# Performance work log

Measured on AMD Instinct MI355X. Metric: run time of the kernel, lower is better.

Reference implementation:

```python
import jax, jax.numpy as jnp
import numpy as np

COMMITMENT_COST = 0.25


def setup_inputs() -> dict:
    key = jax.random.key(0)
    k1, k2 = jax.random.split(key)
    B, S, D, K = 64, 512, 512, 4096
    inputs = jax.random.normal(k1, (B, S, D), dtype=jnp.float32)
    # codebook initialized uniform(-1/K, 1/K) like the torch module
    codebook = jax.random.uniform(k2, (K, D), dtype=jnp.float32,
                                  minval=-1.0 / K, maxval=1.0 / K)
    return {"inputs": inputs, "codebook": codebook}


def reference(inputs, codebook):
    D = inputs.shape[-1]
    flat = inputs.reshape(-1, D)  # [N, D]
    # squared euclidean distances to every code: [N, K]
    dist = (jnp.sum(flat * flat, axis=1, keepdims=True)
            + jnp.sum(codebook * codebook, axis=1)
            - 2.0 * flat @ codebook.T)
    idx = jnp.argmin(dist, axis=1)  # [N]
    # gather replaces one-hot scatter + matmul (same math)
    quantized = codebook[idx].reshape(inputs.shape)
    commitment_loss = jnp.mean((jax.lax.stop_gradient(quantized) - inputs) ** 2)
    codebook_loss = jnp.mean((quantized - jax.lax.stop_gradient(inputs)) ** 2)
    quantize_loss = COMMITMENT_COST * commitment_loss + codebook_loss
    # straight-through estimator
    quantized_st = inputs + jax.lax.stop_gradient(quantized - inputs)
    encoding_indices = idx.reshape(inputs.shape[:-1])
    return quantized_st, quantize_loss, encoding_indices
```

## Files before the change

kernel.cpp:

```cpp
#include <hip/hip_runtime.h>

#define N_ROWS 32768
#define DIM    512
#define KCODES 4096
#define NPARTS 4
#define KPART  (KCODES / NPARTS)
#define Q_ELEMS (N_ROWS * DIM)
#define LOSS_OFF Q_ELEMS
#define IDX_OFF (Q_ELEMS + 1)

__global__ void k_cnorm(const float* __restrict__ cb, float* __restrict__ cnorm) {
    int wave = (blockIdx.x * blockDim.x + threadIdx.x) >> 6;
    int lane = threadIdx.x & 63;
    if (wave >= KCODES) return;
    const float4* row = (const float4*)(cb + (size_t)wave * DIM);
    float4 v1 = row[lane];
    float4 v2 = row[lane + 64];
    float s = v1.x*v1.x + v1.y*v1.y + v1.z*v1.z + v1.w*v1.w
            + v2.x*v2.x + v2.y*v2.y + v2.z*v2.z + v2.w*v2.w;
    #pragma unroll
    for (int m = 32; m >= 1; m >>= 1) s += __shfl_xor(s, m);
    if (lane == 0) cnorm[wave] = s;
}

__global__ void k_xnorm(const float* __restrict__ x, float* __restrict__ xnorm) {
    int wave = (blockIdx.x * blockDim.x + threadIdx.x) >> 6;
    int lane = threadIdx.x & 63;
    if (wave >= N_ROWS) return;
    const float4* row = (const float4*)(x + (size_t)wave * DIM);
    float4 v1 = row[lane];
    float4 v2 = row[lane + 64];
    float s = v1.x*v1.x + v1.y*v1.y + v1.z*v1.z + v1.w*v1.w
            + v2.x*v2.x + v2.y*v2.y + v2.z*v2.z + v2.w*v2.w;
    #pragma unroll
    for (int m = 32; m >= 1; m >>= 1) s += __shfl_xor(s, m);
    if (lane == 0) xnorm[wave] = s;
}

#define BM 64
#define BN 128
#define BD 32
#define NCH ((KPART / BN) * (DIM / BD))

__global__ __launch_bounds__(256)
void k_argmin(const float* __restrict__ x, const float* __restrict__ cb,
              const float* __restrict__ cnorm, const float* __restrict__ xnorm,
              float* __restrict__ bestv, int* __restrict__ bestk) {
    __shared__ float xs[BM][BD + 4];
    __shared__ float cs[BD][BN];

    const int tid = threadIdx.x;
    const int ty = tid >> 4;
    const int tx = tid & 15;
    const int r0 = blockIdx.x * BM;
    const int kbase = blockIdx.y * KPART;

    const int xrow1 = tid >> 3;
    const int xrow2 = (tid + 256) >> 3;
    const int xdq   = tid & 7;
    const int ck    = tid & 127;
    const int cdq0  = tid >> 7;

    float xn[4];
    #pragma unroll
    for (int i = 0; i < 4; ++i) xn[i] = xnorm[r0 + ty * 4 + i];

    float best[4];
    int   bidx[4];
    #pragma unroll
    for (int i = 0; i < 4; ++i) { best[i] = 3.4e38f; bidx[i] = kbase; }

    float acc[4][8];
    float4 xr0, xr1, cr[4];

    xr0 = *(const float4*)(x + (size_t)(r0 + xrow1) * DIM + xdq * 4);
    xr1 = *(const float4*)(x + (size_t)(r0 + xrow2) * DIM + xdq * 4);
    #pragma unroll
    for (int it2 = 0; it2 < 4; ++it2) {
        int dq = cdq0 + it2 * 2;
        cr[it2] = *(const float4*)(cb + (size_t)(kbase + ck) * DIM + dq * 4);
    }

    #pragma unroll 1
    for (int it = 0; it < NCH; ++it) {
        const int kc = it >> 4;

        __syncthreads();
        *(float4*)&xs[xrow1][xdq * 4] = xr0;
        *(float4*)&xs[xrow2][xdq * 4] = xr1;
        #pragma unroll
        for (int it2 = 0; it2 < 4; ++it2) {
            int dq = cdq0 + it2 * 2;
            cs[dq * 4 + 0][ck] = cr[it2].x;
            cs[dq * 4 + 1][ck] = cr[it2].y;
            cs[dq * 4 + 2][ck] = cr[it2].z;
            cs[dq * 4 + 3][ck] = cr[it2].w;
        }
        __syncthreads();

        if (it + 1 < NCH) {
            const int nkc = (it + 1) >> 4;
            const int ndc = ((it + 1) & 15) * BD;
            xr0 = *(const float4*)(x + (size_t)(r0 + xrow1) * DIM + ndc + xdq * 4);
            xr1 = *(const float4*)(x + (size_t)(r0 + xrow2) * DIM + ndc + xdq * 4);
            #pragma unroll
            for (int it2 = 0; it2 < 4; ++it2) {
                int dq = cdq0 + it2 * 2;
                cr[it2] = *(const float4*)(cb + (size_t)(kbase + nkc * BN + ck) * DIM + ndc + dq * 4);
            }
        }

        if ((it & 15) == 0) {
            #pragma unroll
            for (int i = 0; i < 4; ++i)
                #pragma unroll
                for (int j = 0; j < 8; ++j) acc[i][j] = 0.f;
        }

        #pragma unroll
        for (int d4 = 0; d4 < 8; ++d4) {
            float xa[4][4];
            #pragma unroll
            for (int i = 0; i < 4; ++i)
                *(float4*)&xa[i][0] = *(const float4*)&xs[ty * 4 + i][d4 * 4];
            #pragma unroll
            for (int dd = 0; dd < 4; ++dd) {
                int d = d4 * 4 + dd;
                float4 b0 = *(const float4*)&cs[d][tx * 4];
                float4 b1 = *(const float4*)&cs[d][64 + tx * 4];
                #pragma unroll
                for (int i = 0; i < 4; ++i) {
                    float a = xa[i][dd];
                    acc[i][0] = fmaf(a, b0.x, acc[i][0]);
                    acc[i][1] = fmaf(a, b0.y, acc[i][1]);
                    acc[i][2] = fmaf(a, b0.z, acc[i][2]);
                    acc[i][3] = fmaf(a, b0.w, acc[i][3]);
                    acc[i][4] = fmaf(a, b1.x, acc[i][4]);
                    acc[i][5] = fmaf(a, b1.y, acc[i][5]);
                    acc[i][6] = fmaf(a, b1.z, acc[i][6]);
                    acc[i][7] = fmaf(a, b1.w, acc[i][7]);
                }
            }
        }

        if ((it & 15) == 15) {
            #pragma unroll
            for (int half = 0; half < 2; ++half) {
                #pragma unroll
                for (int j = 0; j < 4; ++j) {
                    int k = kbase + kc * BN + half * 64 + tx * 4 + j;
                    float cn = cnorm[k];
                    #pragma unroll
                    for (int i = 0; i < 4; ++i) {
                        float t1 = xn[i] + cn;
                        float tw = 2.0f * acc[i][half * 4 + j];
                        float s  = t1 - tw;
                        if (s < best[i]) { best[i] = s; bidx[i] = k; }
                    }
                }
            }
        }
    }

    #pragma unroll
    for (int i = 0; i < 4; ++i) {
        float b = best[i];
        int   ix = bidx[i];
        #pragma unroll
        for (int m = 1; m <= 8; m <<= 1) {
            float ob = __shfl_xor(b, m);
            int   oi = __shfl_xor(ix, m);
            if (ob < b || (ob == b && oi < ix)) { b = ob; ix = oi; }
        }
        if (tx == 0) {
            int row = r0 + ty * 4 + i;
            bestv[(size_t)blockIdx.y * N_ROWS + row] = b;
            bestk[(size_t)blockIdx.y * N_ROWS + row] = ix;
        }
    }
}

__global__ void k_gather(const float* __restrict__ x, const float* __restrict__ cb,
                         const float* __restrict__ bestv, const int* __restrict__ bestk,
                         float* __restrict__ qout, float* __restrict__ idx_out,
                         float* __restrict__ partial) {
    int row  = blockIdx.x * 4 + (threadIdx.x >> 6);
    int lane = threadIdx.x & 63;
    float bv = bestv[row];
    int   bk = bestk[row];
    #pragma unroll
    for (int p = 1; p < NPARTS; ++p) {
        float v = bestv[(size_t)p * N_ROWS + row];
        int   kk = bestk[(size_t)p * N_ROWS + row];
        if (v < bv) { bv = v; bk = kk; }
    }
    if (lane == 0) idx_out[row] = (float)bk;
    const float4* crow = (const float4*)(cb + (size_t)bk * DIM);
    const float4* xrow = (const float4*)(x + (size_t)row * DIM);
    float4* qrow = (float4*)(qout + (size_t)row * DIM);
    float s = 0.f;
    #pragma unroll
    for (int it = 0; it < 2; ++it) {
        int d4 = lane + it * 64;
        float4 q = crow[d4];
        float4 xi = xrow[d4];
        qrow[d4] = q;
        float dx = q.x - xi.x; s += dx * dx;
        dx = q.y - xi.y; s += dx * dx;
        dx = q.z - xi.z; s += dx * dx;
        dx = q.w - xi.w; s += dx * dx;
    }
    #pragma unroll
    for (int m = 32; m >= 1; m >>= 1) s += __shfl_xor(s, m);
    __shared__ float ws4[4];
    if (lane == 0) ws4[threadIdx.x >> 6] = s;
    __syncthreads();
    if (threadIdx.x == 0)
        partial[blockIdx.x] = (ws4[0] + ws4[1]) + (ws4[2] + ws4[3]);
}

__global__ void k_loss(const float* __restrict__ partial, float* __restrict__ out_loss) {
    int t = threadIdx.x;
    double s = 0.0;
    #pragma unroll 4
    for (int i = 0; i < 32; ++i) s += (double)partial[t * 32 + i];
    #pragma unroll
    for (int m = 32; m >= 1; m >>= 1) s += __shfl_xor(s, m);
    __shared__ double sd[4];
    if ((t & 63) == 0) sd[t >> 6] = s;
    __syncthreads();
    if (t == 0) {
        double tot = (sd[0] + sd[1]) + (sd[2] + sd[3]);
        out_loss[0] = (float)(1.25 * tot / (double)Q_ELEMS);
    }
}

extern "C" void kernel_launch(void* const* d_in, const int* in_sizes, int n_in,
                              void* d_out, int out_size, void* d_ws, size_t ws_size,
                              hipStream_t stream) {
    const float* x  = (const float*)d_in[0];
    const float* cb = (const float*)d_in[1];
    float* out = (float*)d_out;

    char* ws = (char*)d_ws;
    float* cnorm = (float*)ws;                      ws += (size_t)KCODES * 4;
    float* xnorm = (float*)ws;                      ws += (size_t)N_ROWS * 4;
    float* bestv = (float*)ws;                      ws += (size_t)NPARTS * N_ROWS * 4;
    int*   bestk = (int*)ws;                        ws += (size_t)NPARTS * N_ROWS * 4;
    float* part  = (float*)ws;

    k_cnorm<<<KCODES / 4, 256, 0, stream>>>(cb, cnorm);
    k_xnorm<<<N_ROWS / 4, 256, 0, stream>>>(x, xnorm);
    dim3 agrid(N_ROWS / BM, NPARTS);
    k_argmin<<<agrid, 256, 0, stream>>>(x, cb, cnorm, xnorm, bestv, bestk);
    k_gather<<<N_ROWS / 4, 256, 0, stream>>>(x, cb, bestv, bestk, out, out + IDX_OFF, part);
    k_loss<<<1, 256, 0, stream>>>(part, out + LOSS_OFF);
}
```

Baseline: 1.742 ms.

## Halve argmin block threads to 128 with 8x8 per-thread register tile

The distance/argmin kernel now runs 128 threads per block, and each thread computes an 8x8 tile of row-by-code dot products instead of 4x8. Rows are interleaved with stride 8 so each thread reads its x values from shared memory with a different pattern. The register prefetch of the next chunk is removed, so global loads now go straight into shared memory between the two barriers. Doubling per-thread work raises arithmetic intensity per LDS read, but it costs more registers and loses the load/compute overlap that the prefetch gave.

```diff
diff --git a/kernel.cpp b/kernel.cpp
--- a/kernel.cpp
+++ b/kernel.cpp
@@ -40,9 +40,10 @@
 #define BM 64
 #define BN 128
 #define BD 32
+#define NTHR 128
 #define NCH ((KPART / BN) * (DIM / BD))
 
-__global__ __launch_bounds__(256)
+__global__ __launch_bounds__(NTHR)
 void k_argmin(const float* __restrict__ x, const float* __restrict__ cb,
               const float* __restrict__ cnorm, const float* __restrict__ xnorm,
               float* __restrict__ bestv, int* __restrict__ bestk) {
@@ -55,82 +56,66 @@
     const int r0 = blockIdx.x * BM;
     const int kbase = blockIdx.y * KPART;
 
-    const int xrow1 = tid >> 3;
-    const int xrow2 = (tid + 256) >> 3;
-    const int xdq   = tid & 7;
-    const int ck    = tid & 127;
-    const int cdq0  = tid >> 7;
-
-    float xn[4];
-    #pragma unroll
-    for (int i = 0; i < 4; ++i) xn[i] = xnorm[r0 + ty * 4 + i];
-
-    float best[4];
-    int   bidx[4];
-    #pragma unroll
-    for (int i = 0; i < 4; ++i) { best[i] = 3.4e38f; bidx[i] = kbase; }
-
-    float acc[4][8];
-    float4 xr0, xr1, cr[4];
-
-    xr0 = *(const float4*)(x + (size_t)(r0 + xrow1) * DIM + xdq * 4);
-    xr1 = *(const float4*)(x + (size_t)(r0 + xrow2) * DIM + xdq * 4);
-    #pragma unroll
-    for (int it2 = 0; it2 < 4; ++it2) {
-        int dq = cdq0 + it2 * 2;
-        cr[it2] = *(const float4*)(cb + (size_t)(kbase + ck) * DIM + dq * 4);
-    }
+    float xn[8];
+    #pragma unroll
+    for (int i = 0; i < 8; ++i) xn[i] = xnorm[r0 + ty + 8 * i];
+
+    float best[8];
+    int   bidx[8];
+    #pragma unroll
+    for (int i = 0; i < 8; ++i) { best[i] = 3.4e38f; bidx[i] = kbase; }
+
+    float acc[8][8];
 
     #pragma unroll 1
     for (int it = 0; it < NCH; ++it) {
         const int kc = it >> 4;
+        const int dc = (it & 15) * BD;
 
         __syncthreads();
-        *(float4*)&xs[xrow1][xdq * 4] = xr0;
-        *(float4*)&xs[xrow2][xdq * 4] = xr1;
         #pragma unroll
-        for (int it2 = 0; it2 < 4; ++it2) {
-            int dq = cdq0 + it2 * 2;
-            cs[dq * 4 + 0][ck] = cr[it2].x;
-            cs[dq * 4 + 1][ck] = cr[it2].y;
-            cs[dq * 4 + 2][ck] = cr[it2].z;
-            cs[dq * 4 + 3][ck] = cr[it2].w;
+        for (int s = 0; s < 4; ++s) {
+            int f = tid + s * NTHR;
+            int row = f >> 3;
+            int dq  = f & 7;
+            *(float4*)&xs[row][dq * 4] =
+                *(const float4*)(x + (size_t)(r0 + row) * DIM + dc + dq * 4);
+        }
+        {
+            const float* crow = cb + (size_t)(kbase + kc * BN + tid) * DIM + dc;
+            #pragma unroll
+            for (int dq = 0; dq < 8; ++dq) {
+                float4 v = *(const float4*)(crow + dq * 4);
+                cs[dq * 4 + 0][tid] = v.x;
+                cs[dq * 4 + 1][tid] = v.y;
+                cs[dq * 4 + 2][tid] = v.z;
+                cs[dq * 4 + 3][tid] = v.w;
+            }
         }
         __syncthreads();
 
-        if (it + 1 < NCH) {
-            const int nkc = (it + 1) >> 4;
-            const int ndc = ((it + 1) & 15) * BD;
-            xr0 = *(const float4*)(x + (size_t)(r0 + xrow1) * DIM + ndc + xdq * 4);
-            xr1 = *(const float4*)(x + (size_t)(r0 + xrow2) * DIM + ndc + xdq * 4);
-            #pragma unroll
-            for (int it2 = 0; it2 < 4; ++it2) {
-                int dq = cdq0 + it2 * 2;
-                cr[it2] = *(const float4*)(cb + (size_t)(kbase + nkc * BN + ck) * DIM + ndc + dq * 4);
-            }
-        }
-
         if ((it & 15) == 0) {
             #pragma unroll
-            for (int i = 0; i < 4; ++i)
+            for (int i = 0; i < 8; ++i)
                 #pragma unroll
                 for (int j = 0; j < 8; ++j) acc[i][j] = 0.f;
         }
 
         #pragma unroll
         for (int d4 = 0; d4 < 8; ++d4) {
-            float xa[4][4];
-            #pragma unroll
-            for (int i = 0; i < 4; ++i)
-                *(float4*)&xa[i][0] = *(const float4*)&xs[ty * 4 + i][d4 * 4];
+            float4 xa[8];
+            #pragma unroll
+            for (int i = 0; i < 8; ++i)
+                xa[i] = *(const float4*)&xs[ty + 8 * i][d4 * 4];
             #pragma unroll
             for (int dd = 0; dd < 4; ++dd) {
                 int d = d4 * 4 + dd;
                 float4 b0 = *(const float4*)&cs[d][tx * 4];
                 float4 b1 = *(const float4*)&cs[d][64 + tx * 4];
                 #pragma unroll
-                for (int i = 0; i < 4; ++i) {
-                    float a = xa[i][dd];
+                for (int i = 0; i < 8; ++i) {
+                    float a = (dd == 0) ? xa[i].x : (dd == 1) ? xa[i].y
+                            : (dd == 2) ? xa[i].z : xa[i].w;
                     acc[i][0] = fmaf(a, b0.x, acc[i][0]);
                     acc[i][1] = fmaf(a, b0.y, acc[i][1]);
                     acc[i][2] = fmaf(a, b0.z, acc[i][2]);
@@ -151,7 +136,7 @@
                     int k = kbase + kc * BN + half * 64 + tx * 4 + j;
                     float cn = cnorm[k];
                     #pragma unroll
-                    for (int i = 0; i < 4; ++i) {
+                    for (int i = 0; i < 8; ++i) {
                         float t1 = xn[i] + cn;
                         float tw = 2.0f * acc[i][half * 4 + j];
                         float s  = t1 - tw;
@@ -163,7 +148,7 @@
     }
 
     #pragma unroll
-    for (int i = 0; i < 4; ++i) {
+    for (int i = 0; i < 8; ++i) {
         float b = best[i];
         int   ix = bidx[i];
         #pragma unroll
@@ -173,7 +158,7 @@
             if (ob < b || (ob == b && oi < ix)) { b = ob; ix = oi; }
         }
         if (tx == 0) {
-            int row = r0 + ty * 4 + i;
+            int row = r0 + ty + 8 * i;
             bestv[(size_t)blockIdx.y * N_ROWS + row] = b;
             bestk[(size_t)blockIdx.y * N_ROWS + row] = ix;
         }
@@ -252,7 +237,7 @@
     k_cnorm<<<KCODES / 4, 256, 0, stream>>>(cb, cnorm);
     k_xnorm<<<N_ROWS / 4, 256, 0, stream>>>(x, xnorm);
     dim3 agrid(N_ROWS / BM, NPARTS);
-    k_argmin<<<agrid, 256, 0, stream>>>(x, cb, cnorm, xnorm, bestv, bestk);
+    k_argmin<<<agrid, NTHR, 0, stream>>>(x, cb, cnorm, xnorm, bestv, bestk);
     k_gather<<<N_ROWS / 4, 256, 0, stream>>>(x, cb, bestv, bestk, out, out + IDX_OFF, part);
     k_loss<<<1, 256, 0, stream>>>(part, out + LOSS_OFF);
 }
```

After: 1.968 ms. 1.13x slower.
